# Performance work log

Hardware: AMD Instinct MI355X
Metric: run time of the kernel (lower is better)

The kernel has to match this reference:

```python
import jax, jax.numpy as jnp
import numpy as np

N, E = 50000, 800000
IN, HID, OUT = 128, 128, 64
H, ED = 4, 3
D = HID // H  # per-head dim = 32


def _w(key, shape):
    fan_in = shape[-1]
    return jax.random.normal(key, shape, dtype=jnp.float32) / np.sqrt(fan_in)


def setup_inputs() -> dict:
    key = jax.random.key(0)
    ks = jax.random.split(key, 32)
    inp = {
        "x": jax.random.normal(ks[0], (N, IN), dtype=jnp.float32),
        "edge_index": jax.random.randint(ks[1], (2, E), 0, N, dtype=jnp.int32),
        "edge_attr": jax.random.normal(ks[2], (E, ED), dtype=jnp.float32),
        # layer 1 TransformerConv (bias=False)
        "Wq1": _w(ks[3], (HID, IN)), "Wk1": _w(ks[4], (HID, IN)),
        "Wv1": _w(ks[5], (HID, IN)), "We1": _w(ks[6], (HID, ED)),
        "Ws1": _w(ks[7], (HID, IN)),
        # layer 1 MLP [HID,HID,HID]
        "M1a": _w(ks[8], (HID, HID)), "b1a": jnp.zeros((HID,), jnp.float32),
        "M1b": _w(ks[9], (HID, HID)), "b1b": jnp.zeros((HID,), jnp.float32),
        # layer 2 TransformerConv
        "Wq2": _w(ks[10], (HID, HID)), "Wk2": _w(ks[11], (HID, HID)),
        "Wv2": _w(ks[12], (HID, HID)), "We2": _w(ks[13], (HID, ED)),
        "Ws2": _w(ks[14], (HID, HID)),
        # layer 2 MLP
        "M2a": _w(ks[15], (HID, HID)), "b2a": jnp.zeros((HID,), jnp.float32),
        "M2b": _w(ks[16], (HID, HID)), "b2b": jnp.zeros((HID,), jnp.float32),
        # final MLP [HID,HID,OUT], plain_last=False
        "Wf1": _w(ks[17], (HID, HID)), "bf1": jnp.zeros((HID,), jnp.float32),
        "Wf2": _w(ks[18], (OUT, HID)), "bf2": jnp.zeros((OUT,), jnp.float32),
    }
    return inp


def _gelu(x):
    return jax.nn.gelu(x, approximate=True)


def _transformer_conv(x, src, dst, edge_attr, Wq, Wk, Wv, We, Ws, n_nodes):
    # PyG TransformerConv: x_j = x[src] (message source), x_i = x[dst] (target)
    q = (x @ Wq.T).reshape(n_nodes, H, D)
    e = (edge_attr @ We.T).reshape(-1, H, D)              # [E,H,D]
    k = (x @ Wk.T).reshape(n_nodes, H, D)[src] + e        # [E,H,D]
    v = (x @ Wv.T).reshape(n_nodes, H, D)[src] + e        # [E,H,D]
    alpha = jnp.einsum("ehd,ehd->eh", q[dst], k) / jnp.float32(np.sqrt(D))
    # segment softmax over incoming edges of each target node
    m = jax.ops.segment_max(alpha, dst, num_segments=n_nodes)  # [N,H]
    m = jnp.where(jnp.isfinite(m), m, 0.0)
    p = jnp.exp(alpha - m[dst])
    s = jax.ops.segment_sum(p, dst, num_segments=n_nodes)      # [N,H]
    a = p / jnp.maximum(s[dst], 1e-16)                         # [E,H]
    out = jax.ops.segment_sum(a[:, :, None] * v, dst, num_segments=n_nodes)
    out = out.reshape(n_nodes, H * D)
    # root_weight=True (default): skip connection through lin_skip (no bias)
    return out + x @ Ws.T


def _mlp2(x, Wa, ba, Wb, bb):
    # PyG MLP with plain_last=False: act after every linear, norm=None
    h = _gelu(x @ Wa.T + ba)
    return _gelu(h @ Wb.T + bb)


def reference(x, edge_index, edge_attr,
              Wq1, Wk1, Wv1, We1, Ws1, M1a, b1a, M1b, b1b,
              Wq2, Wk2, Wv2, We2, Ws2, M2a, b2a, M2b, b2b,
              Wf1, bf1, Wf2, bf2):
    n_nodes = x.shape[0]
    src, dst = edge_index[0], edge_index[1]
    h = _transformer_conv(x, src, dst, edge_attr, Wq1, Wk1, Wv1, We1, Ws1, n_nodes)
    h = h + _mlp2(h, M1a, b1a, M1b, b1b)
    h = _transformer_conv(h, src, dst, edge_attr, Wq2, Wk2, Wv2, We2, Ws2, n_nodes)
    h = h + _mlp2(h, M2a, b2a, M2b, b2b)
    return _mlp2(h, Wf1, bf1, Wf2, bf2)
```

## Files before the change

### kernel.cpp

```cpp
#include <hip/hip_runtime.h>
#include <hip/hip_bf16.h>
#include <math.h>

#define NN 50000
#define NE 800000
#define NPAD 50048
#define NB_SCAN 196

typedef unsigned short u16;
typedef unsigned int u32;
typedef __attribute__((ext_vector_type(8))) short short8;
typedef __attribute__((ext_vector_type(4))) float float4v;

__device__ __forceinline__ float us2f(u16 u) { return __uint_as_float(((unsigned)u) << 16); }
__device__ __forceinline__ float blo(u32 u) { return __uint_as_float(u << 16); }
__device__ __forceinline__ float bhi(u32 u) { return __uint_as_float(u & 0xffff0000u); }
__device__ __forceinline__ u16 f2us(float f) {
    unsigned x = __float_as_uint(f);
    return (u16)((x + 0x7FFFu + ((x >> 16) & 1u)) >> 16);
}
__device__ __forceinline__ float gelu_f(float x) {
    float p = x * x;
    float t = x * fmaf(p, 0.0713548162726f, 1.5957691216057308f);
    float e = __expf(-t);
    return x * __builtin_amdgcn_rcpf(1.0f + e);
}
__device__ __forceinline__ void lds_fence() {
    asm volatile("s_waitcnt lgkmcnt(0)" ::: "memory");
}

__device__ __forceinline__ float4v mfma4p(const u16* __restrict__ WP, int tile, int l,
                                          short8 a0, short8 a1, short8 a2, short8 a3) {
    const short8* wp = (const short8*)WP + (size_t)tile * 256 + l;
    short8 b0 = wp[0], b1 = wp[64], b2 = wp[128], b3 = wp[192];
    float4v acc = {0.f, 0.f, 0.f, 0.f};
    acc = __builtin_amdgcn_mfma_f32_16x16x32_bf16(a0, b0, acc, 0, 0, 0);
    acc = __builtin_amdgcn_mfma_f32_16x16x32_bf16(a1, b1, acc, 0, 0, 0);
    acc = __builtin_amdgcn_mfma_f32_16x16x32_bf16(a2, b2, acc, 0, 0, 0);
    acc = __builtin_amdgcn_mfma_f32_16x16x32_bf16(a3, b3, acc, 0, 0, 0);
    return acc;
}


__global__ void k_hist(const int* __restrict__ dstv, int* __restrict__ deg) {
    int e = blockIdx.x * blockDim.x + threadIdx.x;
    if (e < NE) atomicAdd(&deg[dstv[e]], 1);
}

__global__ __launch_bounds__(256) void k_scan1(const int* __restrict__ deg,
                                               int* __restrict__ rowstart,
                                               int* __restrict__ bsum) {
    __shared__ int wtot[4];
    int i = blockIdx.x * 256 + threadIdx.x;
    int lane = threadIdx.x & 63, w = threadIdx.x >> 6;
    int v = (i < NN) ? deg[i] : 0;
    int incl = v;
#pragma unroll
    for (int d = 1; d < 64; d <<= 1) {
        int tv = __shfl_up(incl, d);
        if (lane >= d) incl += tv;
    }
    if (lane == 63) wtot[w] = incl;
    __syncthreads();
    if (threadIdx.x == 0) {
        int s = 0;
#pragma unroll
        for (int j = 0; j < 4; ++j) { int t = wtot[j]; wtot[j] = s; s += t; }
        bsum[blockIdx.x] = s;
    }
    __syncthreads();
    if (i < NN) rowstart[i] = incl - v + wtot[w];
}

__global__ __launch_bounds__(256) void k_scan2(int* __restrict__ bsum) {
    __shared__ int wtot[4];
    int t = threadIdx.x;
    int lane = t & 63, w = t >> 6;
    int v = (t < NB_SCAN) ? bsum[t] : 0;
    int incl = v;
#pragma unroll
    for (int d = 1; d < 64; d <<= 1) {
        int tv = __shfl_up(incl, d);
        if (lane >= d) incl += tv;
    }
    if (lane == 63) wtot[w] = incl;
    __syncthreads();
    if (t == 0) {
        int s = 0;
#pragma unroll
        for (int j = 0; j < 4; ++j) { int tt = wtot[j]; wtot[j] = s; s += tt; }
    }
    __syncthreads();
    if (t < NB_SCAN) bsum[t] = incl - v + wtot[w];
}

__global__ void k_scan3(const int* __restrict__ bsum, int* __restrict__ rowstart,
                        int* __restrict__ cursor) {
    int i = blockIdx.x * 256 + threadIdx.x;
    if (i < NN) {
        int v = rowstart[i] + bsum[blockIdx.x];
        rowstart[i] = v;
        cursor[i] = v;
    }
    if (i == 0) rowstart[NN] = NE;
}

__global__ void k_scatter(const int* __restrict__ srcv, const int* __restrict__ dstv,
                          const float* __restrict__ eattr, int* __restrict__ cursor,
                          int4* __restrict__ rec) {
    int e = blockIdx.x * blockDim.x + threadIdx.x;
    if (e >= NE) return;
    int dst = dstv[e];
    int pos = atomicAdd(&cursor[dst], 1);
    int4 r;
    r.x = srcv[e];
    r.y = __float_as_int(eattr[e * 3 + 0]);
    r.z = __float_as_int(eattr[e * 3 + 1]);
    r.w = __float_as_int(eattr[e * 3 + 2]);
    rec[pos] = r;
}


struct CvtEnt { const float* s; u16* d; int n; };
struct CvtTab { CvtEnt e[14]; };
__global__ void k_cvt_w(CvtTab tab) {
    CvtEnt E = tab.e[blockIdx.x >> 3];
    int chunk = blockIdx.x & 7;
    int per = E.n >> 3;
    int lo = chunk * per, hi = lo + per;
    for (int o = lo + threadIdx.x; o < hi; o += blockDim.x) {
        int tile = o >> 11;
        int q = (o >> 9) & 3;
        int l = (o >> 3) & 63;
        int j = o & 7;
        int row = tile * 16 + (l & 15);
        int col = q * 32 + (l >> 4) * 8 + j;
        E.d[o] = f2us(E.s[row * 128 + col]);
    }
}


__device__ __forceinline__ void stage_plain(u16* buf, int kb, int m, int tt, float4v acc) {
#pragma unroll
    for (int r = 0; r < 4; ++r) buf[(kb * 4 + r) * 136 + tt * 16 + m] = f2us(acc[r]);
}
__device__ __forceinline__ void store128(const u16* buf, u16* dst, int r0w, int coff, int l) {
#pragma unroll
    for (int it = 0; it < 4; ++it) {
        int j = it * 64 + l;
        int row = j >> 4, col = (j & 15) * 8;
        *(uint4*)(dst + (size_t)(r0w + row) * 512 + coff + col) = *(const uint4*)&buf[row * 136 + col];
    }
}
__device__ __forceinline__ void read_frags(const u16* buf, int m, int kb,
                                           short8& f0, short8& f1, short8& f2, short8& f3) {
    const u16* p = buf + m * 136 + kb * 8;
    f0 = *(const short8*)(p);
    f1 = *(const short8*)(p + 32);
    f2 = *(const short8*)(p + 64);
    f3 = *(const short8*)(p + 96);
}


__global__ __launch_bounds__(256, 4) void k_qkvs1(const float* __restrict__ Ain,
                                                  const u16* __restrict__ W,
                                                  u16* __restrict__ QKVS) {
    __shared__ u16 tile[4][16 * 136];
    int tid = threadIdx.x;
    int l = tid & 63, w = tid >> 6, m = l & 15, kb = l >> 4;
    int r0w = blockIdx.x * 64 + w * 16;
    u16* my = tile[w];

    short8 a0, a1, a2, a3;
    {
        const float* ap = Ain + (size_t)(r0w + m) * 128;
        bool ok = (r0w + m) < NN;
        short8* dsts[4] = {&a0, &a1, &a2, &a3};
#pragma unroll
        for (int i = 0; i < 4; ++i) {
            short8 r;
            if (ok) {
                const float* p = ap + (kb + i * 4) * 8;
                float4 f0 = *(const float4*)p;
                float4 f1 = *(const float4*)(p + 4);
                r[0]=(short)f2us(f0.x); r[1]=(short)f2us(f0.y); r[2]=(short)f2us(f0.z); r[3]=(short)f2us(f0.w);
                r[4]=(short)f2us(f1.x); r[5]=(short)f2us(f1.y); r[6]=(short)f2us(f1.z); r[7]=(short)f2us(f1.w);
            } else {
#pragma unroll
                for (int j = 0; j < 8; ++j) r[j] = 0;
            }
            *dsts[i] = r;
        }
    }

#pragma unroll
    for (int tt = 0; tt < 8; ++tt) stage_plain(my, kb, m, tt, mfma4p(W, tt, l, a0, a1, a2, a3));
    lds_fence();
    store128(my, QKVS, r0w, 0, l);
    lds_fence();
#pragma unroll
    for (int tt = 0; tt < 4; ++tt) {
        float4v acc = mfma4p(W, 8 + tt, l, a0, a1, a2, a3);
        int c = tt * 32 + 8 * (m >> 2) + (m & 3);
#pragma unroll
        for (int r = 0; r < 4; ++r) my[(kb * 4 + r) * 136 + c] = f2us(acc[r]);
    }
#pragma unroll
    for (int tt = 0; tt < 4; ++tt) {
        float4v acc = mfma4p(W, 16 + tt, l, a0, a1, a2, a3);
        int c = tt * 32 + 8 * (m >> 2) + (m & 3) + 4;
#pragma unroll
        for (int r = 0; r < 4; ++r) my[(kb * 4 + r) * 136 + c] = f2us(acc[r]);
    }
    lds_fence();
    store128(my, QKVS, r0w, 128, l);
    lds_fence();
#pragma unroll
    for (int tt = 0; tt < 4; ++tt) {
        float4v acc = mfma4p(W, 12 + tt, l, a0, a1, a2, a3);
        int c = tt * 32 + 8 * (m >> 2) + (m & 3);
#pragma unroll
        for (int r = 0; r < 4; ++r) my[(kb * 4 + r) * 136 + c] = f2us(acc[r]);
    }
#pragma unroll
    for (int tt = 0; tt < 4; ++tt) {
        float4v acc = mfma4p(W, 20 + tt, l, a0, a1, a2, a3);
        int c = tt * 32 + 8 * (m >> 2) + (m & 3) + 4;
#pragma unroll
        for (int r = 0; r < 4; ++r) my[(kb * 4 + r) * 136 + c] = f2us(acc[r]);
    }
    lds_fence();
    store128(my, QKVS, r0w, 256, l);
    lds_fence();
#pragma unroll
    for (int tt = 0; tt < 8; ++tt) stage_plain(my, kb, m, tt, mfma4p(W, 24 + tt, l, a0, a1, a2, a3));
    lds_fence();
    store128(my, QKVS, r0w, 384, l);
}


__global__ __launch_bounds__(256, 4) void k_mlp_qkvs(const u16* __restrict__ Ain,
                                                     const u16* __restrict__ Wm,
                                                     const float* __restrict__ bias1,
                                                     const float* __restrict__ bias2,
                                                     const u16* __restrict__ Wq,
                                                     u16* __restrict__ QKVS) {
    __shared__ u16 shb[4][16 * 136];
    __shared__ u16 t1b[4][16 * 136];
    int tid = threadIdx.x;
    int l = tid & 63, w = tid >> 6, m = l & 15, kb = l >> 4;
    int r0w = blockIdx.x * 64 + w * 16;
    u16* sh = shb[w];
    u16* t1 = t1b[w];

    const short8* arow = (const short8*)(Ain + (size_t)(r0w + m) * 128);
    short8 a0 = arow[kb], a1 = arow[kb + 4], a2 = arow[kb + 8], a3 = arow[kb + 12];
    {
        u16* p = sh + m * 136 + kb * 8;
        *(short8*)(p) = a0;
        *(short8*)(p + 32) = a1;
        *(short8*)(p + 64) = a2;
        *(short8*)(p + 96) = a3;
    }
#pragma unroll
    for (int tt = 0; tt < 8; ++tt) {
        float4v acc = mfma4p(Wm, tt, l, a0, a1, a2, a3);
        float bv = bias1[tt * 16 + m];
#pragma unroll
        for (int r = 0; r < 4; ++r)
            t1[(kb * 4 + r) * 136 + tt * 16 + m] = f2us(gelu_f(acc[r] + bv));
    }
    lds_fence();
    short8 c0, c1, c2, c3;
    read_frags(t1, m, kb, c0, c1, c2, c3);
#pragma unroll
    for (int tt = 0; tt < 8; ++tt) {
        float4v acc = mfma4p(Wm + 16384, tt, l, c0, c1, c2, c3);
        float bv = bias2[tt * 16 + m];
#pragma unroll
        for (int r = 0; r < 4; ++r) {
            int idx = (kb * 4 + r) * 136 + tt * 16 + m;
            sh[idx] = f2us(gelu_f(acc[r] + bv) + us2f(sh[idx]));
        }
    }
    lds_fence();
    short8 h0, h1, h2, h3;
    read_frags(sh, m, kb, h0, h1, h2, h3);

#pragma unroll
    for (int tt = 0; tt < 8; ++tt) stage_plain(t1, kb, m, tt, mfma4p(Wq, tt, l, h0, h1, h2, h3));
    lds_fence();
    store128(t1, QKVS, r0w, 0, l);
    lds_fence();
#pragma unroll
    for (int tt = 0; tt < 4; ++tt) {
        float4v acc = mfma4p(Wq, 8 + tt, l, h0, h1, h2, h3);
        int c = tt * 32 + 8 * (m >> 2) + (m & 3);
#pragma unroll
        for (int r = 0; r < 4; ++r) t1[(kb * 4 + r) * 136 + c] = f2us(acc[r]);
    }
#pragma unroll
    for (int tt = 0; tt < 4; ++tt) {
        float4v acc = mfma4p(Wq, 16 + tt, l, h0, h1, h2, h3);
        int c = tt * 32 + 8 * (m >> 2) + (m & 3) + 4;
#pragma unroll
        for (int r = 0; r < 4; ++r) t1[(kb * 4 + r) * 136 + c] = f2us(acc[r]);
    }
    lds_fence();
    store128(t1, QKVS, r0w, 128, l);
    lds_fence();
#pragma unroll
    for (int tt = 0; tt < 4; ++tt) {
        float4v acc = mfma4p(Wq, 12 + tt, l, h0, h1, h2, h3);
        int c = tt * 32 + 8 * (m >> 2) + (m & 3);
#pragma unroll
        for (int r = 0; r < 4; ++r) t1[(kb * 4 + r) * 136 + c] = f2us(acc[r]);
    }
#pragma unroll
    for (int tt = 0; tt < 4; ++tt) {
        float4v acc = mfma4p(Wq, 20 + tt, l, h0, h1, h2, h3);
        int c = tt * 32 + 8 * (m >> 2) + (m & 3) + 4;
#pragma unroll
        for (int r = 0; r < 4; ++r) t1[(kb * 4 + r) * 136 + c] = f2us(acc[r]);
    }
    lds_fence();
    store128(t1, QKVS, r0w, 256, l);
    lds_fence();
#pragma unroll
    for (int tt = 0; tt < 8; ++tt) stage_plain(t1, kb, m, tt, mfma4p(Wq, 24 + tt, l, h0, h1, h2, h3));
    lds_fence();
    store128(t1, QKVS, r0w, 384, l);
}


__global__ __launch_bounds__(256, 4) void k_mlp_final(const u16* __restrict__ Ain,
                                                      const u16* __restrict__ Wm,
                                                      const float* __restrict__ bias1,
                                                      const float* __restrict__ bias2,
                                                      const u16* __restrict__ Wf,
                                                      const float* __restrict__ bf1,
                                                      const float* __restrict__ bf2,
                                                      float* __restrict__ outp) {
    __shared__ u16 shb[4][16 * 136];
    __shared__ u16 t1b[4][16 * 136];
    int tid = threadIdx.x;
    int l = tid & 63, w = tid >> 6, m = l & 15, kb = l >> 4;
    int r0w = blockIdx.x * 64 + w * 16;
    u16* sh = shb[w];
    u16* t1 = t1b[w];

    const short8* arow = (const short8*)(Ain + (size_t)(r0w + m) * 128);
    short8 a0 = arow[kb], a1 = arow[kb + 4], a2 = arow[kb + 8], a3 = arow[kb + 12];
    {
        u16* p = sh + m * 136 + kb * 8;
        *(short8*)(p) = a0;
        *(short8*)(p + 32) = a1;
        *(short8*)(p + 64) = a2;
        *(short8*)(p + 96) = a3;
    }
#pragma unroll
    for (int tt = 0; tt < 8; ++tt) {
        float4v acc = mfma4p(Wm, tt, l, a0, a1, a2, a3);
        float bv = bias1[tt * 16 + m];
#pragma unroll
        for (int r = 0; r < 4; ++r)
            t1[(kb * 4 + r) * 136 + tt * 16 + m] = f2us(gelu_f(acc[r] + bv));
    }
    lds_fence();
    short8 c0, c1, c2, c3;
    read_frags(t1, m, kb, c0, c1, c2, c3);
#pragma unroll
    for (int tt = 0; tt < 8; ++tt) {
        float4v acc = mfma4p(Wm + 16384, tt, l, c0, c1, c2, c3);
        float bv = bias2[tt * 16 + m];
#pragma unroll
        for (int r = 0; r < 4; ++r) {
            int idx = (kb * 4 + r) * 136 + tt * 16 + m;
            sh[idx] = f2us(gelu_f(acc[r] + bv) + us2f(sh[idx]));
        }
    }
    lds_fence();
    short8 h0, h1, h2, h3;
    read_frags(sh, m, kb, h0, h1, h2, h3);
#pragma unroll
    for (int tt = 0; tt < 8; ++tt) {
        float4v acc = mfma4p(Wf, tt, l, h0, h1, h2, h3);
        float bv = bf1[tt * 16 + m];
#pragma unroll
        for (int r = 0; r < 4; ++r)
            t1[(kb * 4 + r) * 136 + tt * 16 + m] = f2us(gelu_f(acc[r] + bv));
    }
    lds_fence();
    short8 f0, f1, f2, f3;
    read_frags(t1, m, kb, f0, f1, f2, f3);
    lds_fence();
#pragma unroll
    for (int tt = 0; tt < 4; ++tt) {
        float4v acc = mfma4p(Wf + 16384, tt, l, f0, f1, f2, f3);
        float bv = bf2[tt * 16 + m];
#pragma unroll
        for (int r = 0; r < 4; ++r)
            t1[(kb * 4 + r) * 136 + tt * 16 + m] = f2us(gelu_f(acc[r] + bv));
    }
    lds_fence();
#pragma unroll
    for (int it = 0; it < 2; ++it) {
        int j = it * 64 + l;
        int row = j >> 3, col = (j & 7) * 8;
        int grow = r0w + row;
        if (grow < NN) {
            uint4 pk = *(const uint4*)&t1[row * 136 + col];
            const u16* pv = (const u16*)&pk;
            float* po = outp + (size_t)grow * 64 + col;
            float4 o0 = {us2f(pv[0]), us2f(pv[1]), us2f(pv[2]), us2f(pv[3])};
            float4 o1 = {us2f(pv[4]), us2f(pv[5]), us2f(pv[6]), us2f(pv[7])};
            *(float4*)po = o0;
            *(float4*)(po + 4) = o1;
        }
    }
}


__global__ __launch_bounds__(256) void k_conv(const int* __restrict__ rowstart,
                                              const int4* __restrict__ rec,
                                              const u16* __restrict__ qkvs,
                                              const float* __restrict__ We,
                                              u16* __restrict__ out) {
    int n = blockIdx.x * 4 + (threadIdx.x >> 6);
    int l = threadIdx.x & 63;
    int half = l >> 5;
    int li = l & 31;
    int c0 = (li >> 3) * 32 + (li & 7) * 4;
    const u16* qrow = qkvs + (size_t)n * 512;
    uint2 qu = *(const uint2*)(qrow + c0);
    float q0 = blo(qu.x), q1 = bhi(qu.x), q2 = blo(qu.y), q3 = bhi(qu.y);
    float w00 = We[c0 * 3 + 0], w01 = We[c0 * 3 + 1], w02 = We[c0 * 3 + 2];
    float w10 = We[c0 * 3 + 3], w11 = We[c0 * 3 + 4], w12 = We[c0 * 3 + 5];
    float w20 = We[c0 * 3 + 6], w21 = We[c0 * 3 + 7], w22 = We[c0 * 3 + 8];
    float w30 = We[c0 * 3 + 9], w31 = We[c0 * 3 + 10], w32 = We[c0 * 3 + 11];
    float g0 = fmaf(q3, w30, fmaf(q2, w20, fmaf(q1, w10, q0 * w00)));
    float g1 = fmaf(q3, w31, fmaf(q2, w21, fmaf(q1, w11, q0 * w01)));
    float g2 = fmaf(q3, w32, fmaf(q2, w22, fmaf(q1, w12, q0 * w02)));
#pragma unroll
    for (int d = 1; d <= 4; d <<= 1) {
        g0 += __shfl_xor(g0, d);
        g1 += __shfl_xor(g1, d);
        g2 += __shfl_xor(g2, d);
    }
    int e0 = rowstart[n], e1 = rowstart[n + 1];
    float ss = 0.f, o0 = 0.f, o1 = 0.f, o2 = 0.f, o3 = 0.f, S0 = 0.f, S1 = 0.f, S2 = 0.f;
    int kvoff = 128 + li * 8;

    auto edge = [&](int4 r, uint4 kv) {
        float part = fmaf(q3, bhi(kv.y), fmaf(q2, blo(kv.y), fmaf(q1, bhi(kv.x), q0 * blo(kv.x))));
        part += __shfl_xor(part, 1);
        part += __shfl_xor(part, 2);
        part += __shfl_xor(part, 4);
        float ea0 = __int_as_float(r.y), ea1 = __int_as_float(r.z), ea2 = __int_as_float(r.w);
        float alpha = fmaf(ea2, g2, fmaf(ea1, g1, fmaf(ea0, g0, part))) * 0.17677669529663687f;
        float p = __expf(fminf(alpha, 80.f));
        o0 = fmaf(p, blo(kv.z), o0);
        o1 = fmaf(p, bhi(kv.z), o1);
        o2 = fmaf(p, blo(kv.w), o2);
        o3 = fmaf(p, bhi(kv.w), o3);
        ss += p;
        S0 = fmaf(p, ea0, S0);
        S1 = fmaf(p, ea1, S1);
        S2 = fmaf(p, ea2, S2);
    };

    int e = e0 + half;
    int cnt = (e < e1) ? ((e1 - e + 1) >> 1) : 0;
    if (cnt & 1) {
        int4 r = rec[e];
        uint4 kv = *(const uint4*)(qkvs + (size_t)r.x * 512 + kvoff);
        edge(r, kv);
        e += 2;
    }
    for (int i = 0; i < (cnt >> 1); ++i, e += 4) {
        int4 ra = rec[e], rb = rec[e + 2];
        uint4 kva = *(const uint4*)(qkvs + (size_t)ra.x * 512 + kvoff);
        uint4 kvb = *(const uint4*)(qkvs + (size_t)rb.x * 512 + kvoff);
        edge(ra, kva);
        edge(rb, kvb);
    }
    o0 += __shfl_xor(o0, 32);
    o1 += __shfl_xor(o1, 32);
    o2 += __shfl_xor(o2, 32);
    o3 += __shfl_xor(o3, 32);
    ss += __shfl_xor(ss, 32);
    S0 += __shfl_xor(S0, 32);
    S1 += __shfl_xor(S1, 32);
    S2 += __shfl_xor(S2, 32);
    if (half == 0) {
        float inv = __builtin_amdgcn_rcpf(fmaxf(ss, 1e-16f));
        o0 = fmaf(w02, S2, fmaf(w01, S1, fmaf(w00, S0, o0)));
        o1 = fmaf(w12, S2, fmaf(w11, S1, fmaf(w10, S0, o1)));
        o2 = fmaf(w22, S2, fmaf(w21, S1, fmaf(w20, S0, o2)));
        o3 = fmaf(w32, S2, fmaf(w31, S1, fmaf(w30, S0, o3)));
        uint2 su = *(const uint2*)(qrow + 384 + c0);
        float r0v = fmaf(o0, inv, blo(su.x));
        float r1v = fmaf(o1, inv, bhi(su.x));
        float r2v = fmaf(o2, inv, blo(su.y));
        float r3v = fmaf(o3, inv, bhi(su.y));
        uint2 ou;
        ou.x = (u32)f2us(r0v) | ((u32)f2us(r1v) << 16);
        ou.y = (u32)f2us(r2v) | ((u32)f2us(r3v) << 16);
        *(uint2*)(out + (size_t)n * 128 + c0) = ou;
    }
}


extern "C" void kernel_launch(void* const* d_in, const int* in_sizes, int n_in,
                              void* d_out, int out_size, void* d_ws, size_t ws_size,
                              hipStream_t stream) {
    const float* x = (const float*)d_in[0];
    const int* ei = (const int*)d_in[1];
    const float* eattr = (const float*)d_in[2];
    const float* Wq1 = (const float*)d_in[3];
    const float* Wk1 = (const float*)d_in[4];
    const float* Wv1 = (const float*)d_in[5];
    const float* We1 = (const float*)d_in[6];
    const float* Ws1 = (const float*)d_in[7];
    const float* M1a = (const float*)d_in[8];
    const float* b1a = (const float*)d_in[9];
    const float* M1b = (const float*)d_in[10];
    const float* b1b = (const float*)d_in[11];
    const float* Wq2 = (const float*)d_in[12];
    const float* Wk2 = (const float*)d_in[13];
    const float* Wv2 = (const float*)d_in[14];
    const float* We2 = (const float*)d_in[15];
    const float* Ws2 = (const float*)d_in[16];
    const float* M2a = (const float*)d_in[17];
    const float* b2a = (const float*)d_in[18];
    const float* M2b = (const float*)d_in[19];
    const float* b2b = (const float*)d_in[20];
    const float* Wf1 = (const float*)d_in[21];
    const float* bf1 = (const float*)d_in[22];
    const float* Wf2 = (const float*)d_in[23];
    const float* bf2 = (const float*)d_in[24];

    char* ws = (char*)d_ws;
    size_t off = 0;
    auto alloc = [&](size_t bytes) -> void* {
        void* p = ws + off;
        off = (off + bytes + 255) & ~(size_t)255;
        return p;
    };
    int* deg = (int*)alloc((size_t)NN * 4);
    int* rowstart = (int*)alloc((size_t)(NN + 1) * 4);
    int* cursor = (int*)alloc((size_t)NN * 4);
    int* bsum = (int*)alloc((size_t)NB_SCAN * 4);
    int4* rec = (int4*)alloc((size_t)NE * 16);
    u16* QKVS = (u16*)alloc((size_t)NPAD * 512 * 2);
    u16* Ha = (u16*)alloc((size_t)NPAD * 128 * 2);
    u16* WB[14];
    const int wsz[14] = {16384, 16384, 16384, 16384, 16384, 16384, 16384,
                         16384, 16384, 16384, 16384, 16384, 16384, 8192};
    for (int i = 0; i < 14; ++i) WB[i] = (u16*)alloc((size_t)wsz[i] * 2);

    const int* srcv = ei;
    const int* dstv = ei + NE;

    hipMemsetAsync(deg, 0, (size_t)NN * 4, stream);
    k_hist<<<(NE + 255) / 256, 256, 0, stream>>>(dstv, deg);
    k_scan1<<<NB_SCAN, 256, 0, stream>>>(deg, rowstart, bsum);
    k_scan2<<<1, 256, 0, stream>>>(bsum);
    k_scan3<<<NB_SCAN, 256, 0, stream>>>(bsum, rowstart, cursor);
    k_scatter<<<(NE + 255) / 256, 256, 0, stream>>>(srcv, dstv, eattr, cursor, rec);

    CvtTab tab;
    const float* wsrc[14] = {Wq1, Wk1, Wv1, Ws1, Wq2, Wk2, Wv2, Ws2,
                             M1a, M1b, M2a, M2b, Wf1, Wf2};
    for (int i = 0; i < 14; ++i) { tab.e[i].s = wsrc[i]; tab.e[i].d = WB[i]; tab.e[i].n = wsz[i]; }
    k_cvt_w<<<112, 256, 0, stream>>>(tab);

    dim3 blk(256);
    dim3 grd(NPAD / 64);
    dim3 gconv(NN / 4);

    k_qkvs1<<<grd, blk, 0, stream>>>(x, WB[0], QKVS);
    k_conv<<<gconv, blk, 0, stream>>>(rowstart, rec, QKVS, We1, Ha);
    k_mlp_qkvs<<<grd, blk, 0, stream>>>(Ha, WB[8], b1a, b1b, WB[4], QKVS);
    k_conv<<<gconv, blk, 0, stream>>>(rowstart, rec, QKVS, We2, Ha);
    k_mlp_final<<<grd, blk, 0, stream>>>(Ha, WB[10], b2a, b2b, WB[12], bf1, bf2, (float*)d_out);
}
```

Baseline: 410.1 us.

## Split QKVS projection across two grid halves and rework conv edge loop

The QKV/skip projection kernels now launch with a second grid dimension, so each block computes half of the output columns. This doubles parallelism, at the cost of k_mlp_qkvs recomputing its MLP prefix in both halves. The conv kernel now has each wave process four edges at once, with 16 lanes per edge and 8 channels per lane. It software-pipelines the next record and K/V loads, pre-scales q, and uses vectorized loads of the edge weights. The aim is to hide gather latency and cut shuffle work, in exchange for more registers and the duplicated MLP compute.

```diff
diff --git a/kernel.cpp b/kernel.cpp
--- a/kernel.cpp
+++ b/kernel.cpp
@@ -162,6 +162,7 @@
 }
 
 
+
 __global__ __launch_bounds__(256, 4) void k_qkvs1(const float* __restrict__ Ain,
                                                   const u16* __restrict__ W,
                                                   u16* __restrict__ QKVS) {
@@ -193,49 +194,51 @@
         }
     }
 
-#pragma unroll
-    for (int tt = 0; tt < 8; ++tt) stage_plain(my, kb, m, tt, mfma4p(W, tt, l, a0, a1, a2, a3));
-    lds_fence();
-    store128(my, QKVS, r0w, 0, l);
-    lds_fence();
-#pragma unroll
-    for (int tt = 0; tt < 4; ++tt) {
-        float4v acc = mfma4p(W, 8 + tt, l, a0, a1, a2, a3);
-        int c = tt * 32 + 8 * (m >> 2) + (m & 3);
-#pragma unroll
-        for (int r = 0; r < 4; ++r) my[(kb * 4 + r) * 136 + c] = f2us(acc[r]);
-    }
-#pragma unroll
-    for (int tt = 0; tt < 4; ++tt) {
-        float4v acc = mfma4p(W, 16 + tt, l, a0, a1, a2, a3);
-        int c = tt * 32 + 8 * (m >> 2) + (m & 3) + 4;
-#pragma unroll
-        for (int r = 0; r < 4; ++r) my[(kb * 4 + r) * 136 + c] = f2us(acc[r]);
-    }
-    lds_fence();
-    store128(my, QKVS, r0w, 128, l);
-    lds_fence();
-#pragma unroll
-    for (int tt = 0; tt < 4; ++tt) {
-        float4v acc = mfma4p(W, 12 + tt, l, a0, a1, a2, a3);
-        int c = tt * 32 + 8 * (m >> 2) + (m & 3);
-#pragma unroll
-        for (int r = 0; r < 4; ++r) my[(kb * 4 + r) * 136 + c] = f2us(acc[r]);
-    }
-#pragma unroll
-    for (int tt = 0; tt < 4; ++tt) {
-        float4v acc = mfma4p(W, 20 + tt, l, a0, a1, a2, a3);
-        int c = tt * 32 + 8 * (m >> 2) + (m & 3) + 4;
-#pragma unroll
-        for (int r = 0; r < 4; ++r) my[(kb * 4 + r) * 136 + c] = f2us(acc[r]);
-    }
-    lds_fence();
-    store128(my, QKVS, r0w, 256, l);
-    lds_fence();
-#pragma unroll
-    for (int tt = 0; tt < 8; ++tt) stage_plain(my, kb, m, tt, mfma4p(W, 24 + tt, l, a0, a1, a2, a3));
-    lds_fence();
-    store128(my, QKVS, r0w, 384, l);
+    if (blockIdx.y == 0) {
+#pragma unroll
+        for (int tt = 0; tt < 8; ++tt) stage_plain(my, kb, m, tt, mfma4p(W, tt, l, a0, a1, a2, a3));
+        lds_fence();
+        store128(my, QKVS, r0w, 0, l);
+        lds_fence();
+#pragma unroll
+        for (int tt = 0; tt < 4; ++tt) {
+            float4v acc = mfma4p(W, 8 + tt, l, a0, a1, a2, a3);
+            int c = tt * 32 + 8 * (m >> 2) + (m & 3);
+#pragma unroll
+            for (int r = 0; r < 4; ++r) my[(kb * 4 + r) * 136 + c] = f2us(acc[r]);
+        }
+#pragma unroll
+        for (int tt = 0; tt < 4; ++tt) {
+            float4v acc = mfma4p(W, 16 + tt, l, a0, a1, a2, a3);
+            int c = tt * 32 + 8 * (m >> 2) + (m & 3) + 4;
+#pragma unroll
+            for (int r = 0; r < 4; ++r) my[(kb * 4 + r) * 136 + c] = f2us(acc[r]);
+        }
+        lds_fence();
+        store128(my, QKVS, r0w, 128, l);
+    } else {
+#pragma unroll
+        for (int tt = 0; tt < 4; ++tt) {
+            float4v acc = mfma4p(W, 12 + tt, l, a0, a1, a2, a3);
+            int c = tt * 32 + 8 * (m >> 2) + (m & 3);
+#pragma unroll
+            for (int r = 0; r < 4; ++r) my[(kb * 4 + r) * 136 + c] = f2us(acc[r]);
+        }
+#pragma unroll
+        for (int tt = 0; tt < 4; ++tt) {
+            float4v acc = mfma4p(W, 20 + tt, l, a0, a1, a2, a3);
+            int c = tt * 32 + 8 * (m >> 2) + (m & 3) + 4;
+#pragma unroll
+            for (int r = 0; r < 4; ++r) my[(kb * 4 + r) * 136 + c] = f2us(acc[r]);
+        }
+        lds_fence();
+        store128(my, QKVS, r0w, 256, l);
+        lds_fence();
+#pragma unroll
+        for (int tt = 0; tt < 8; ++tt) stage_plain(my, kb, m, tt, mfma4p(W, 24 + tt, l, a0, a1, a2, a3));
+        lds_fence();
+        store128(my, QKVS, r0w, 384, l);
+    }
 }
 
 
@@ -287,49 +290,51 @@
     short8 h0, h1, h2, h3;
     read_frags(sh, m, kb, h0, h1, h2, h3);
 
-#pragma unroll
-    for (int tt = 0; tt < 8; ++tt) stage_plain(t1, kb, m, tt, mfma4p(Wq, tt, l, h0, h1, h2, h3));
-    lds_fence();
-    store128(t1, QKVS, r0w, 0, l);
-    lds_fence();
-#pragma unroll
-    for (int tt = 0; tt < 4; ++tt) {
-        float4v acc = mfma4p(Wq, 8 + tt, l, h0, h1, h2, h3);
-        int c = tt * 32 + 8 * (m >> 2) + (m & 3);
-#pragma unroll
-        for (int r = 0; r < 4; ++r) t1[(kb * 4 + r) * 136 + c] = f2us(acc[r]);
-    }
-#pragma unroll
-    for (int tt = 0; tt < 4; ++tt) {
-        float4v acc = mfma4p(Wq, 16 + tt, l, h0, h1, h2, h3);
-        int c = tt * 32 + 8 * (m >> 2) + (m & 3) + 4;
-#pragma unroll
-        for (int r = 0; r < 4; ++r) t1[(kb * 4 + r) * 136 + c] = f2us(acc[r]);
-    }
-    lds_fence();
-    store128(t1, QKVS, r0w, 128, l);
-    lds_fence();
-#pragma unroll
-    for (int tt = 0; tt < 4; ++tt) {
-        float4v acc = mfma4p(Wq, 12 + tt, l, h0, h1, h2, h3);
-        int c = tt * 32 + 8 * (m >> 2) + (m & 3);
-#pragma unroll
-        for (int r = 0; r < 4; ++r) t1[(kb * 4 + r) * 136 + c] = f2us(acc[r]);
-    }
-#pragma unroll
-    for (int tt = 0; tt < 4; ++tt) {
-        float4v acc = mfma4p(Wq, 20 + tt, l, h0, h1, h2, h3);
-        int c = tt * 32 + 8 * (m >> 2) + (m & 3) + 4;
-#pragma unroll
-        for (int r = 0; r < 4; ++r) t1[(kb * 4 + r) * 136 + c] = f2us(acc[r]);
-    }
-    lds_fence();
-    store128(t1, QKVS, r0w, 256, l);
-    lds_fence();
-#pragma unroll
-    for (int tt = 0; tt < 8; ++tt) stage_plain(t1, kb, m, tt, mfma4p(Wq, 24 + tt, l, h0, h1, h2, h3));
-    lds_fence();
-    store128(t1, QKVS, r0w, 384, l);
+    if (blockIdx.y == 0) {
+#pragma unroll
+        for (int tt = 0; tt < 8; ++tt) stage_plain(t1, kb, m, tt, mfma4p(Wq, tt, l, h0, h1, h2, h3));
+        lds_fence();
+        store128(t1, QKVS, r0w, 0, l);
+        lds_fence();
+#pragma unroll
+        for (int tt = 0; tt < 4; ++tt) {
+            float4v acc = mfma4p(Wq, 8 + tt, l, h0, h1, h2, h3);
+            int c = tt * 32 + 8 * (m >> 2) + (m & 3);
+#pragma unroll
+            for (int r = 0; r < 4; ++r) t1[(kb * 4 + r) * 136 + c] = f2us(acc[r]);
+        }
+#pragma unroll
+        for (int tt = 0; tt < 4; ++tt) {
+            float4v acc = mfma4p(Wq, 16 + tt, l, h0, h1, h2, h3);
+            int c = tt * 32 + 8 * (m >> 2) + (m & 3) + 4;
+#pragma unroll
+            for (int r = 0; r < 4; ++r) t1[(kb * 4 + r) * 136 + c] = f2us(acc[r]);
+        }
+        lds_fence();
+        store128(t1, QKVS, r0w, 128, l);
+    } else {
+#pragma unroll
+        for (int tt = 0; tt < 4; ++tt) {
+            float4v acc = mfma4p(Wq, 12 + tt, l, h0, h1, h2, h3);
+            int c = tt * 32 + 8 * (m >> 2) + (m & 3);
+#pragma unroll
+            for (int r = 0; r < 4; ++r) t1[(kb * 4 + r) * 136 + c] = f2us(acc[r]);
+        }
+#pragma unroll
+        for (int tt = 0; tt < 4; ++tt) {
+            float4v acc = mfma4p(Wq, 20 + tt, l, h0, h1, h2, h3);
+            int c = tt * 32 + 8 * (m >> 2) + (m & 3) + 4;
+#pragma unroll
+            for (int r = 0; r < 4; ++r) t1[(kb * 4 + r) * 136 + c] = f2us(acc[r]);
+        }
+        lds_fence();
+        store128(t1, QKVS, r0w, 256, l);
+        lds_fence();
+#pragma unroll
+        for (int tt = 0; tt < 8; ++tt) stage_plain(t1, kb, m, tt, mfma4p(Wq, 24 + tt, l, h0, h1, h2, h3));
+        lds_fence();
+        store128(t1, QKVS, r0w, 384, l);
+    }
 }
 
 
@@ -428,85 +433,112 @@
                                               u16* __restrict__ out) {
     int n = blockIdx.x * 4 + (threadIdx.x >> 6);
     int l = threadIdx.x & 63;
-    int half = l >> 5;
-    int li = l & 31;
-    int c0 = (li >> 3) * 32 + (li & 7) * 4;
+    int quarter = l >> 4;
+    int li = l & 15;
+    int c0 = li * 8;
     const u16* qrow = qkvs + (size_t)n * 512;
-    uint2 qu = *(const uint2*)(qrow + c0);
-    float q0 = blo(qu.x), q1 = bhi(qu.x), q2 = blo(qu.y), q3 = bhi(qu.y);
-    float w00 = We[c0 * 3 + 0], w01 = We[c0 * 3 + 1], w02 = We[c0 * 3 + 2];
-    float w10 = We[c0 * 3 + 3], w11 = We[c0 * 3 + 4], w12 = We[c0 * 3 + 5];
-    float w20 = We[c0 * 3 + 6], w21 = We[c0 * 3 + 7], w22 = We[c0 * 3 + 8];
-    float w30 = We[c0 * 3 + 9], w31 = We[c0 * 3 + 10], w32 = We[c0 * 3 + 11];
-    float g0 = fmaf(q3, w30, fmaf(q2, w20, fmaf(q1, w10, q0 * w00)));
-    float g1 = fmaf(q3, w31, fmaf(q2, w21, fmaf(q1, w11, q0 * w01)));
-    float g2 = fmaf(q3, w32, fmaf(q2, w22, fmaf(q1, w12, q0 * w02)));
-#pragma unroll
-    for (int d = 1; d <= 4; d <<= 1) {
-        g0 += __shfl_xor(g0, d);
-        g1 += __shfl_xor(g1, d);
-        g2 += __shfl_xor(g2, d);
-    }
+    uint4 qu = *(const uint4*)(qrow + c0);
+    const float SC = 0.17677669529663687f;
+    float q0 = blo(qu.x) * SC, q1 = bhi(qu.x) * SC, q2 = blo(qu.y) * SC, q3 = bhi(qu.y) * SC;
+    float q4 = blo(qu.z) * SC, q5 = bhi(qu.z) * SC, q6 = blo(qu.w) * SC, q7 = bhi(qu.w) * SC;
+    const float* wep = We + c0 * 3;
+    float g0, g1, g2;
+    {
+        float4 w0 = *(const float4*)(wep);
+        float4 w1 = *(const float4*)(wep + 4);
+        float4 w2 = *(const float4*)(wep + 8);
+        float4 w3 = *(const float4*)(wep + 12);
+        float4 w4 = *(const float4*)(wep + 16);
+        float4 w5 = *(const float4*)(wep + 20);
+        g0 = q0*w0.x + q1*w0.w + q2*w1.z + q3*w2.y + q4*w3.x + q5*w3.w + q6*w4.z + q7*w5.y;
+        g1 = q0*w0.y + q1*w1.x + q2*w1.w + q3*w2.z + q4*w3.y + q5*w4.x + q6*w4.w + q7*w5.z;
+        g2 = q0*w0.z + q1*w1.y + q2*w2.x + q3*w2.w + q4*w3.z + q5*w4.y + q6*w5.x + q7*w5.w;
+    }
+    g0 += __shfl_xor(g0, 1); g1 += __shfl_xor(g1, 1); g2 += __shfl_xor(g2, 1);
+    g0 += __shfl_xor(g0, 2); g1 += __shfl_xor(g1, 2); g2 += __shfl_xor(g2, 2);
+
     int e0 = rowstart[n], e1 = rowstart[n + 1];
-    float ss = 0.f, o0 = 0.f, o1 = 0.f, o2 = 0.f, o3 = 0.f, S0 = 0.f, S1 = 0.f, S2 = 0.f;
-    int kvoff = 128 + li * 8;
-
-    auto edge = [&](int4 r, uint4 kv) {
-        float part = fmaf(q3, bhi(kv.y), fmaf(q2, blo(kv.y), fmaf(q1, bhi(kv.x), q0 * blo(kv.x))));
-        part += __shfl_xor(part, 1);
-        part += __shfl_xor(part, 2);
-        part += __shfl_xor(part, 4);
-        float ea0 = __int_as_float(r.y), ea1 = __int_as_float(r.z), ea2 = __int_as_float(r.w);
-        float alpha = fmaf(ea2, g2, fmaf(ea1, g1, fmaf(ea0, g0, part))) * 0.17677669529663687f;
-        float p = __expf(fminf(alpha, 80.f));
-        o0 = fmaf(p, blo(kv.z), o0);
-        o1 = fmaf(p, bhi(kv.z), o1);
-        o2 = fmaf(p, blo(kv.w), o2);
-        o3 = fmaf(p, bhi(kv.w), o3);
-        ss += p;
-        S0 = fmaf(p, ea0, S0);
-        S1 = fmaf(p, ea1, S1);
-        S2 = fmaf(p, ea2, S2);
-    };
-
-    int e = e0 + half;
-    int cnt = (e < e1) ? ((e1 - e + 1) >> 1) : 0;
-    if (cnt & 1) {
-        int4 r = rec[e];
-        uint4 kv = *(const uint4*)(qkvs + (size_t)r.x * 512 + kvoff);
-        edge(r, kv);
-        e += 2;
-    }
-    for (int i = 0; i < (cnt >> 1); ++i, e += 4) {
-        int4 ra = rec[e], rb = rec[e + 2];
-        uint4 kva = *(const uint4*)(qkvs + (size_t)ra.x * 512 + kvoff);
-        uint4 kvb = *(const uint4*)(qkvs + (size_t)rb.x * 512 + kvoff);
-        edge(ra, kva);
-        edge(rb, kvb);
-    }
-    o0 += __shfl_xor(o0, 32);
-    o1 += __shfl_xor(o1, 32);
-    o2 += __shfl_xor(o2, 32);
-    o3 += __shfl_xor(o3, 32);
-    ss += __shfl_xor(ss, 32);
-    S0 += __shfl_xor(S0, 32);
-    S1 += __shfl_xor(S1, 32);
-    S2 += __shfl_xor(S2, 32);
-    if (half == 0) {
-        float inv = __builtin_amdgcn_rcpf(fmaxf(ss, 1e-16f));
-        o0 = fmaf(w02, S2, fmaf(w01, S1, fmaf(w00, S0, o0)));
-        o1 = fmaf(w12, S2, fmaf(w11, S1, fmaf(w10, S0, o1)));
-        o2 = fmaf(w22, S2, fmaf(w21, S1, fmaf(w20, S0, o2)));
-        o3 = fmaf(w32, S2, fmaf(w31, S1, fmaf(w30, S0, o3)));
-        uint2 su = *(const uint2*)(qrow + 384 + c0);
-        float r0v = fmaf(o0, inv, blo(su.x));
-        float r1v = fmaf(o1, inv, bhi(su.x));
-        float r2v = fmaf(o2, inv, blo(su.y));
-        float r3v = fmaf(o3, inv, bhi(su.y));
-        uint2 ou;
+    int deg = e1 - e0;
+    float ss = 0.f, S0 = 0.f, S1 = 0.f, S2 = 0.f;
+    float o0 = 0.f, o1 = 0.f, o2 = 0.f, o3 = 0.f, o4 = 0.f, o5 = 0.f, o6 = 0.f, o7 = 0.f;
+
+    if (deg > 0) {
+        int iters = (deg + 3) >> 2;
+        int eb = e0 + quarter;
+        int elast = e1 - 1;
+        int4 r0 = rec[min(eb, elast)];
+        int4 r1 = rec[min(eb + 4, elast)];
+        const u16* kvB = qkvs + 128 + (size_t)li * 16;
+        uint4 kA = *(const uint4*)(kvB + (size_t)r0.x * 512);
+        uint4 kB = *(const uint4*)(kvB + (size_t)r0.x * 512 + 8);
+        for (int i = 0; i < iters; ++i) {
+            int4 r2 = rec[min(eb + 4 * (i + 2), elast)];
+            const u16* kp = kvB + (size_t)r1.x * 512;
+            uint4 nA = *(const uint4*)(kp);
+            uint4 nB = *(const uint4*)(kp + 8);
+            float part = q0 * blo(kA.x) + q1 * bhi(kA.x) + q2 * blo(kA.y) + q3 * bhi(kA.y)
+                       + q4 * blo(kB.x) + q5 * bhi(kB.x) + q6 * blo(kB.y) + q7 * bhi(kB.y);
+            part += __shfl_xor(part, 1);
+            part += __shfl_xor(part, 2);
+            float ea0 = __int_as_float(r0.y), ea1 = __int_as_float(r0.z), ea2 = __int_as_float(r0.w);
+            float alpha = fmaf(ea2, g2, fmaf(ea1, g1, fmaf(ea0, g0, part)));
+            float p = __expf(fminf(alpha, 80.f));
+            p = (eb + 4 * i < e1) ? p : 0.f;
+            o0 = fmaf(p, blo(kA.z), o0);
+            o1 = fmaf(p, bhi(kA.z), o1);
+            o2 = fmaf(p, blo(kA.w), o2);
+            o3 = fmaf(p, bhi(kA.w), o3);
+            o4 = fmaf(p, blo(kB.z), o4);
+            o5 = fmaf(p, bhi(kB.z), o5);
+            o6 = fmaf(p, blo(kB.w), o6);
+            o7 = fmaf(p, bhi(kB.w), o7);
+            ss += p;
+            S0 = fmaf(p, ea0, S0);
+            S1 = fmaf(p, ea1, S1);
+            S2 = fmaf(p, ea2, S2);
+            r0 = r1; r1 = r2; kA = nA; kB = nB;
+        }
+    }
+    o0 += __shfl_xor(o0, 16); o1 += __shfl_xor(o1, 16); o2 += __shfl_xor(o2, 16); o3 += __shfl_xor(o3, 16);
+    o4 += __shfl_xor(o4, 16); o5 += __shfl_xor(o5, 16); o6 += __shfl_xor(o6, 16); o7 += __shfl_xor(o7, 16);
+    ss += __shfl_xor(ss, 16); S0 += __shfl_xor(S0, 16); S1 += __shfl_xor(S1, 16); S2 += __shfl_xor(S2, 16);
+    o0 += __shfl_xor(o0, 32); o1 += __shfl_xor(o1, 32); o2 += __shfl_xor(o2, 32); o3 += __shfl_xor(o3, 32);
+    o4 += __shfl_xor(o4, 32); o5 += __shfl_xor(o5, 32); o6 += __shfl_xor(o6, 32); o7 += __shfl_xor(o7, 32);
+    ss += __shfl_xor(ss, 32); S0 += __shfl_xor(S0, 32); S1 += __shfl_xor(S1, 32); S2 += __shfl_xor(S2, 32);
+
+    float inv = __builtin_amdgcn_rcpf(fmaxf(ss, 1e-16f));
+    {
+        float4 w0 = *(const float4*)(wep);
+        float4 w1 = *(const float4*)(wep + 4);
+        float4 w2 = *(const float4*)(wep + 8);
+        float4 w3 = *(const float4*)(wep + 12);
+        float4 w4 = *(const float4*)(wep + 16);
+        float4 w5 = *(const float4*)(wep + 20);
+        o0 += w0.x * S0 + w0.y * S1 + w0.z * S2;
+        o1 += w0.w * S0 + w1.x * S1 + w1.y * S2;
+        o2 += w1.z * S0 + w1.w * S1 + w2.x * S2;
+        o3 += w2.y * S0 + w2.z * S1 + w2.w * S2;
+        o4 += w3.x * S0 + w3.y * S1 + w3.z * S2;
+        o5 += w3.w * S0 + w4.x * S1 + w4.y * S2;
+        o6 += w4.z * S0 + w4.w * S1 + w5.x * S2;
+        o7 += w5.y * S0 + w5.z * S1 + w5.w * S2;
+    }
+    uint4 su = *(const uint4*)(qrow + 384 + c0);
+    float r0v = fmaf(o0, inv, blo(su.x));
+    float r1v = fmaf(o1, inv, bhi(su.x));
+    float r2v = fmaf(o2, inv, blo(su.y));
+    float r3v = fmaf(o3, inv, bhi(su.y));
+    float r4v = fmaf(o4, inv, blo(su.z));
+    float r5v = fmaf(o5, inv, bhi(su.z));
+    float r6v = fmaf(o6, inv, blo(su.w));
+    float r7v = fmaf(o7, inv, bhi(su.w));
+    if (quarter == 0) {
+        uint4 ou;
         ou.x = (u32)f2us(r0v) | ((u32)f2us(r1v) << 16);
         ou.y = (u32)f2us(r2v) | ((u32)f2us(r3v) << 16);
-        *(uint2*)(out + (size_t)n * 128 + c0) = ou;
+        ou.z = (u32)f2us(r4v) | ((u32)f2us(r5v) << 16);
+        ou.w = (u32)f2us(r6v) | ((u32)f2us(r7v) << 16);
+        *(uint4*)(out + (size_t)n * 128 + c0) = ou;
     }
 }
 
@@ -576,12 +608,13 @@
     k_cvt_w<<<112, 256, 0, stream>>>(tab);
 
     dim3 blk(256);
+    dim3 grd2(NPAD / 64, 2);
     dim3 grd(NPAD / 64);
     dim3 gconv(NN / 4);
 
-    k_qkvs1<<<grd, blk, 0, stream>>>(x, WB[0], QKVS);
+    k_qkvs1<<<grd2, blk, 0, stream>>>(x, WB[0], QKVS);
     k_conv<<<gconv, blk, 0, stream>>>(rowstart, rec, QKVS, We1, Ha);
-    k_mlp_qkvs<<<grd, blk, 0, stream>>>(Ha, WB[8], b1a, b1b, WB[4], QKVS);
+    k_mlp_qkvs<<<grd2, blk, 0, stream>>>(Ha, WB[8], b1a, b1b, WB[4], QKVS);
     k_conv<<<gconv, blk, 0, stream>>>(rowstart, rec, QKVS, We2, Ha);
     k_mlp_final<<<grd, blk, 0, stream>>>(Ha, WB[10], b2a, b2b, WB[12], bf1, bf2, (float*)d_out);
 }
```

New measurement: 419.7 us. +2.4%, slower.
